# Optimization experiments

Hardware: AMD Instinct MI355X
Metric: run time of the kernel (lower is better)

Reference implementation:

```python
import jax, jax.numpy as jnp
from jax import lax
import numpy as np

V, E, H, T, L = 100000, 300, 512, 11, 4096
START, STOP = 9, 10
NEG_INF = -10000.0


def setup_inputs() -> dict:
    key = jax.random.key(0)
    ks = jax.random.split(key, 14)
    n = lambda k, s, sc=0.1: jax.random.normal(k, s, dtype=jnp.float32) * sc
    transitions = jax.random.normal(ks[12], (T, T), dtype=jnp.float32)
    # __init__ pins transitions into START and out of STOP
    transitions = transitions.at[START, :].set(NEG_INF).at[:, STOP].set(NEG_INF)
    return {
        'sentence': jax.random.randint(ks[0], (L,), 0, V),
        'embedding': n(ks[1], (V, E), 1.0),
        'w_ih_f': n(ks[2], (4 * H, E)), 'w_hh_f': n(ks[3], (4 * H, H)),
        'b_ih_f': n(ks[4], (4 * H,)), 'b_hh_f': n(ks[5], (4 * H,)),
        'w_ih_b': n(ks[6], (4 * H, E)), 'w_hh_b': n(ks[7], (4 * H, H)),
        'b_ih_b': n(ks[8], (4 * H,)), 'b_hh_b': n(ks[9], (4 * H,)),
        'w_tag': n(ks[10], (T, 2 * H)), 'b_tag': n(ks[11], (T,)),
        'transitions': transitions,
    }


def _lstm(x, w_ih, w_hh, b_ih, b_hh, reverse):
    # x: [L, E]; PyTorch gate order i, f, g, o
    Hd = w_hh.shape[1]
    # precompute input projections for all timesteps: [L, 4H]
    xg = x @ w_ih.T + b_ih + b_hh
    def step(carry, xt):
        h, c = carry
        g = xt + w_hh @ h
        i, f, gg, o = jnp.split(g, 4)
        c = jax.nn.sigmoid(f) * c + jax.nn.sigmoid(i) * jnp.tanh(gg)
        h = jax.nn.sigmoid(o) * jnp.tanh(c)
        return (h, c), h
    init = (jnp.zeros((Hd,), x.dtype), jnp.zeros((Hd,), x.dtype))
    _, hs = lax.scan(step, init, xg, reverse=reverse)
    return hs  # [L, H]


def _get_lstm_features(sentence, embedding, w_ih_f, w_hh_f, b_ih_f, b_hh_f,
                       w_ih_b, w_hh_b, b_ih_b, b_hh_b, w_tag, b_tag):
    x = embedding[sentence]  # [L, E]
    hf = _lstm(x, w_ih_f, w_hh_f, b_ih_f, b_hh_f, reverse=False)
    hb = _lstm(x, w_ih_b, w_hh_b, b_ih_b, b_hh_b, reverse=True)
    h = jnp.concatenate([hf, hb], axis=-1)  # [L, 2H]
    return h @ w_tag.T + b_tag  # [L, T]


def _viterbi(feats, transitions):
    init = jnp.full((T,), NEG_INF, feats.dtype).at[START].set(0.0)
    def step(fv, feat):
        scores = fv[None, :] + transitions  # [T_next, T_prev]
        bptr = jnp.argmax(scores, axis=1)
        fv2 = jnp.max(scores, axis=1) + feat
        return fv2, bptr
    fv, bptrs = lax.scan(step, init, feats)  # bptrs: [L, T]
    terminal = fv + transitions[STOP]
    best = jnp.argmax(terminal)
    path_score = terminal[best]
    def back(tag, bp):
        return bp[tag], tag
    _, path = lax.scan(back, best, bptrs, reverse=True)  # tags for t=0..L-1
    return path_score, path


def reference(sentence, embedding, w_ih_f, w_hh_f, b_ih_f, b_hh_f,
              w_ih_b, w_hh_b, b_ih_b, b_hh_b, w_tag, b_tag, transitions):
    feats = _get_lstm_features(sentence, embedding, w_ih_f, w_hh_f, b_ih_f, b_hh_f,
                               w_ih_b, w_hh_b, b_ih_b, b_hh_b, w_tag, b_tag)
    return _viterbi(feats, transitions)
```

## Files before the change

kernel.cpp:

```cpp
#include <hip/hip_runtime.h>
#include <hip/hip_bf16.h>
#include <hip/hip_fp16.h>
#include <stdint.h>

#define LL 4096
#define EE 300
#define HH 512
#define G4H 2048
#define TT 11
#define TSTART 9
#define TSTOP 10
#define NEGINF -10000.0f

typedef unsigned long long u64;
typedef _Float16 h2v __attribute__((ext_vector_type(2)));

__device__ __forceinline__ float sigf(float x){
    x = fminf(fmaxf(x, -30.f), 30.f);
    return 1.0f / (1.0f + __expf(-x));
}
__device__ __forceinline__ float tanhfast(float x){
    x = fminf(fmaxf(x, -15.f), 15.f);
    float e = __expf(-2.0f * x);
    return (1.0f - e) / (1.0f + e);
}
__device__ __forceinline__ u64 lda(const u64* p){
    return __hip_atomic_load(p, __ATOMIC_RELAXED, __HIP_MEMORY_SCOPE_AGENT);
}
__device__ __forceinline__ h2v u2h(unsigned u){
    union { unsigned v; h2v h; } c; c.v = u; return c.h;
}
__device__ __forceinline__ h2v pk(float a, float b){
    auto r = __builtin_amdgcn_cvt_pkrtz(a, b);
    union { decltype(r) x; h2v h; } c; c.x = r; return c.h;
}

__global__ void k0_zero(u64* __restrict__ comm){
    int i = blockIdx.x * blockDim.x + threadIdx.x;
    if (i < 2 * 2 * HH) comm[i] = 0ull;
}

__global__ __launch_bounds__(256) void k1_xg(
    const int* __restrict__ sent, const float* __restrict__ emb,
    const float* __restrict__ wih_f, const float* __restrict__ bih_f, const float* __restrict__ bhh_f,
    const float* __restrict__ wih_b, const float* __restrict__ bih_b, const float* __restrict__ bhh_b,
    float* __restrict__ xg_f, float* __restrict__ xg_b)
{
    __shared__ float elds[32 * 304];
    int t0  = blockIdx.x * 32;
    int r0  = blockIdx.y * 256;
    int dir = blockIdx.z;
    const float* wih = dir ? wih_b : wih_f;
    const float* bih = dir ? bih_b : bih_f;
    const float* bhh = dir ? bhh_b : bhh_f;
    float* xg = dir ? xg_b : xg_f;

    for (int idx = threadIdx.x; idx < 32 * EE; idx += 256){
        int i = idx / EE, e = idx - i * EE;
        elds[i * 304 + e] = emb[(long)sent[t0 + i] * EE + e];
    }
    __syncthreads();

    int rA = r0 + (threadIdx.x & 127);
    int rB = rA + 128;
    int half = threadIdx.x >> 7;
    float accA[16], accB[16];
    #pragma unroll
    for (int i = 0; i < 16; i++){ accA[i] = 0.f; accB[i] = 0.f; }
    const float* wrowA = wih + (long)rA * EE;
    const float* wrowB = wih + (long)rB * EE;
    for (int e4 = 0; e4 < 75; e4++){
        float4 wa = *reinterpret_cast<const float4*>(wrowA + e4 * 4);
        float4 wb = *reinterpret_cast<const float4*>(wrowB + e4 * 4);
        #pragma unroll
        for (int i = 0; i < 16; i++){
            float4 ev = *reinterpret_cast<const float4*>(&elds[(half * 16 + i) * 304 + e4 * 4]);
            accA[i] += wa.x * ev.x + wa.y * ev.y + wa.z * ev.z + wa.w * ev.w;
            accB[i] += wb.x * ev.x + wb.y * ev.y + wb.z * ev.z + wb.w * ev.w;
        }
    }
    float bA = bih[rA] + bhh[rA];
    float bB = bih[rB] + bhh[rB];
    #pragma unroll
    for (int i = 0; i < 16; i++){
        int t = t0 + half * 16 + i;
        xg[(long)t * G4H + rA] = accA[i] + bA;
        xg[(long)t * G4H + rB] = accB[i] + bB;
    }
}

__global__ __launch_bounds__(512) void k2_lstm(
    const float* __restrict__ whh_f, const float* __restrict__ whh_b,
    const float* __restrict__ xg_f, const float* __restrict__ xg_b,
    float* __restrict__ hs_f, float* __restrict__ hs_b,
    u64* __restrict__ comm)
{
    int dir = blockIdx.x >> 5;
    int b   = blockIdx.x & 31;
    int j0  = b * 16;
    int tid = threadIdx.x;
    int w   = tid >> 6;
    int l   = tid & 63;
    int g   = l >> 4;
    int jl  = l & 15;
    int row = g * HH + j0 + jl;

    const float* whh = dir ? whh_b : whh_f;
    const float* xg  = dir ? xg_b  : xg_f;
    float* hs        = dir ? hs_b  : hs_f;
    u64* cm          = comm + dir * 2 * HH;

    h2v wreg[32];
    {
        const float* wp = whh + (size_t)row * HH + w * 64;
        #pragma unroll
        for (int m = 0; m < 32; m += 2){
            float4 v = *reinterpret_cast<const float4*>(wp + 2 * m);
            wreg[m]     = pk(v.x, v.y);
            wreg[m + 1] = pk(v.z, v.w);
        }
    }

    __shared__ __align__(16) unsigned short hl16[2][HH];
    __shared__ float plds[2][512];
    float c = 0.f;

    for (int s = 0; s < LL; ++s){
        int t = dir ? (LL - 1 - s) : s;
        float xgv = 0.f;
        if (tid < 64) xgv = xg[(size_t)t * G4H + row];

        if (s == 0){
            hl16[0][tid] = 0;
        } else {
            const u64* pw = cm + (s & 1) * HH + tid;
            u64 v = lda(pw);
            unsigned want = (unsigned)s;
            while (!__all((unsigned)(v >> 32) == want)){
                if ((unsigned)(v >> 32) != want) v = lda(pw);
            }
            float hval = __uint_as_float((unsigned)v);
            union { h2v h; unsigned u; } cv2; cv2.h = pk(hval, hval);
            hl16[s & 1][tid] = (unsigned short)(cv2.u & 0xFFFFu);
        }
        __syncthreads();

        float a0 = 0.f, a1 = 0.f, a2 = 0.f, a3 = 0.f;
        {
            const uint4* hseg = reinterpret_cast<const uint4*>(&hl16[s & 1][w * 64]);
            #pragma unroll
            for (int q = 0; q < 8; q += 2){
                uint4 h0 = hseg[q];
                uint4 h1 = hseg[q + 1];
                a0 = __builtin_amdgcn_fdot2(wreg[4*q+0], u2h(h0.x), a0, false);
                a1 = __builtin_amdgcn_fdot2(wreg[4*q+1], u2h(h0.y), a1, false);
                a2 = __builtin_amdgcn_fdot2(wreg[4*q+2], u2h(h0.z), a2, false);
                a3 = __builtin_amdgcn_fdot2(wreg[4*q+3], u2h(h0.w), a3, false);
                a0 = __builtin_amdgcn_fdot2(wreg[4*q+4], u2h(h1.x), a0, false);
                a1 = __builtin_amdgcn_fdot2(wreg[4*q+5], u2h(h1.y), a1, false);
                a2 = __builtin_amdgcn_fdot2(wreg[4*q+6], u2h(h1.z), a2, false);
                a3 = __builtin_amdgcn_fdot2(wreg[4*q+7], u2h(h1.w), a3, false);
            }
        }
        plds[s & 1][tid] = (a0 + a1) + (a2 + a3);
        __syncthreads();

        if (w == 0){
            float sum = 0.f;
            #pragma unroll
            for (int q = 0; q < 8; q++) sum += plds[s & 1][q * 64 + l];
            float pre = sum + xgv;
            float vi = __shfl(pre, jl,      64);
            float vf = __shfl(pre, 16 + jl, 64);
            float vg = __shfl(pre, 32 + jl, 64);
            float vo = __shfl(pre, 48 + jl, 64);
            c = sigf(vf) * c + sigf(vi) * tanhfast(vg);
            float h = sigf(vo) * tanhfast(c);
            if (l < 16){
                union { float f; unsigned u; } hv; hv.f = h;
                u64 pk2 = ((u64)(s + 1) << 32) | (u64)hv.u;
                __hip_atomic_store(cm + ((s + 1) & 1) * HH + (j0 + l), pk2,
                                   __ATOMIC_RELAXED, __HIP_MEMORY_SCOPE_AGENT);
                hs[(size_t)t * HH + (j0 + l)] = h;
            }
        }
    }
}

__global__ __launch_bounds__(64) void k3_feats(
    const float* __restrict__ hs_f, const float* __restrict__ hs_b,
    const float* __restrict__ wtag, const float* __restrict__ btag,
    float* __restrict__ feats)
{
    int t = blockIdx.x;
    int lane = threadIdx.x;
    float hreg[16];
    #pragma unroll
    for (int q = 0; q < 16; q++){
        int k = q * 64 + lane;
        hreg[q] = (q < 8) ? hs_f[(long)t * HH + k] : hs_b[(long)t * HH + (k - HH)];
    }
    for (int n = 0; n < TT; n++){
        float a = 0.f;
        #pragma unroll
        for (int q = 0; q < 16; q++){
            a += wtag[n * 1024 + q * 64 + lane] * hreg[q];
        }
        #pragma unroll
        for (int off = 32; off; off >>= 1) a += __shfl_down(a, off, 64);
        if (lane == 0) feats[t * 12 + n] = a + btag[n];
    }
}

__global__ __launch_bounds__(64) void k4a_chunk(
    const float* __restrict__ feats, const float* __restrict__ trans,
    float* __restrict__ Pmat)
{
    int c = blockIdx.x;
    int lane = threadIdx.x;
    float tr[TT][TT];
    #pragma unroll
    for (int n = 0; n < TT; n++)
        #pragma unroll
        for (int p = 0; p < TT; p++) tr[n][p] = trans[n * TT + p];

    float pv[TT];
    #pragma unroll
    for (int n = 0; n < TT; n++) pv[n] = (n == lane) ? 0.f : NEGINF;

    for (int i = 0; i < 64; i++){
        int t = c * 64 + i;
        float ft[TT];
        #pragma unroll
        for (int n = 0; n < TT; n++) ft[n] = feats[t * 12 + n];
        float pn[TT];
        #pragma unroll
        for (int n = 0; n < TT; n++){
            float m = tr[n][0] + pv[0];
            #pragma unroll
            for (int p = 1; p < TT; p++) m = fmaxf(m, tr[n][p] + pv[p]);
            pn[n] = m + ft[n];
        }
        #pragma unroll
        for (int n = 0; n < TT; n++) pv[n] = pn[n];
    }
    if (lane < TT){
        #pragma unroll
        for (int n = 0; n < TT; n++) Pmat[(c * TT + n) * TT + lane] = pv[n];
    }
}

__global__ __launch_bounds__(64) void k4b_bound(
    const float* __restrict__ Pmat, float* __restrict__ fvb)
{
    int lane = threadIdx.x;
    int ln = (lane < TT) ? lane : 0;
    float fv[TT];
    #pragma unroll
    for (int n = 0; n < TT; n++) fv[n] = (n == TSTART) ? 0.f : NEGINF;

    for (int c = 0; c < 64; c++){
        if (lane < TT) fvb[c * TT + lane] = fv[lane];
        float nf = NEGINF;
        #pragma unroll
        for (int s = 0; s < TT; s++)
            nf = fmaxf(nf, Pmat[(c * TT + ln) * TT + s] + fv[s]);
        #pragma unroll
        for (int n = 0; n < TT; n++) fv[n] = __shfl(nf, n, 64);
    }
    if (lane < TT) fvb[64 * TT + lane] = fv[lane];
}

__global__ __launch_bounds__(64) void k4c_bp(
    const float* __restrict__ feats, const float* __restrict__ trans,
    const float* __restrict__ fvb, u64* __restrict__ bpw)
{
    int c = blockIdx.x;
    int lane = threadIdx.x;
    int ln = (lane < TT) ? lane : 0;
    float trl[TT];
    #pragma unroll
    for (int p = 0; p < TT; p++) trl[p] = trans[ln * TT + p];
    float fv[TT];
    #pragma unroll
    for (int n = 0; n < TT; n++) fv[n] = fvb[c * TT + n];

    for (int i = 0; i < 64; i++){
        int t = c * 64 + i;
        float best = NEGINF; int bp = 0;
        #pragma unroll
        for (int p = 0; p < TT; p++){
            float sp = trl[p] + fv[p];
            if (sp > best){ best = sp; bp = p; }
        }
        if (lane >= TT) bp = 0;
        unsigned lo = (lane < 8) ? ((unsigned)bp << (4 * lane)) : 0u;
        unsigned hi = (lane >= 8 && lane < TT) ? ((unsigned)bp << (4 * (lane - 8))) : 0u;
        #pragma unroll
        for (int off = 1; off < 16; off <<= 1){
            lo |= __shfl_xor(lo, off, 16); hi |= __shfl_xor(hi, off, 16);
        }
        if (lane == 0) bpw[t] = (u64)lo | ((u64)hi << 32);
        float nf = (lane < TT) ? best + feats[t * 12 + ln] : NEGINF;
        #pragma unroll
        for (int n = 0; n < TT; n++) fv[n] = __shfl(nf, n, 64);
    }
}

__global__ __launch_bounds__(256) void k4d_bt(
    const u64* __restrict__ bpw, const float* __restrict__ fvb,
    const float* __restrict__ trans, float* __restrict__ out)
{
    __shared__ u64 bl[LL];
    int tid = threadIdx.x;
    for (int i = tid; i < LL; i += 256) bl[i] = bpw[i];
    __syncthreads();

    if (tid < 64){
        int lane = tid;
        int ln = (lane < TT) ? lane : 0;
        float term = (lane < TT) ? (fvb[64 * TT + ln] + trans[TSTOP * TT + ln]) : -3.0e38f;
        int idx = (lane < TT) ? lane : 63;
        #pragma unroll
        for (int off = 32; off; off >>= 1){
            float os = __shfl_down(term, off, 64);
            int   oi = __shfl_down(idx,  off, 64);
            if (os > term || (os == term && oi < idx)){ term = os; idx = oi; }
        }
        if (lane == 0){
            out[0] = term;
            int tag = idx;
            out[1 + (LL - 1)] = (float)tag;
            for (int u = LL - 1; u >= 1; --u){
                tag = (int)((bl[u] >> (4 * tag)) & 15ull);
                out[u] = (float)tag;
            }
        }
    }
}

__global__ void k_dbg(float* out, float v){ out[0] = v; }

extern "C" void kernel_launch(void* const* d_in, const int* in_sizes, int n_in,
                              void* d_out, int out_size, void* d_ws, size_t ws_size,
                              hipStream_t stream)
{
    const int*   sent  = (const int*)  d_in[0];
    const float* emb   = (const float*)d_in[1];
    const float* wih_f = (const float*)d_in[2];
    const float* whh_f = (const float*)d_in[3];
    const float* bih_f = (const float*)d_in[4];
    const float* bhh_f = (const float*)d_in[5];
    const float* wih_b = (const float*)d_in[6];
    const float* whh_b = (const float*)d_in[7];
    const float* bih_b = (const float*)d_in[8];
    const float* bhh_b = (const float*)d_in[9];
    const float* wtag  = (const float*)d_in[10];
    const float* btag  = (const float*)d_in[11];
    const float* trans = (const float*)d_in[12];
    float* out = (float*)d_out;

    char* ws = (char*)d_ws;
    size_t off = 0;
    float* xg_f = (float*)(ws + off); off += (size_t)LL * G4H * 4;
    float* xg_b = (float*)(ws + off); off += (size_t)LL * G4H * 4;
    float* hs_f = (float*)(ws + off); off += (size_t)LL * HH * 4;
    float* hs_b = (float*)(ws + off); off += (size_t)LL * HH * 4;
    float* feats= (float*)(ws + off); off += (size_t)LL * 12 * 4;
    u64* comm   = (u64*)(ws + off);   off += 2 * 2 * HH * 8;
    float* Pmat = (float*)(ws + off); off += (size_t)64 * TT * TT * 4;
    float* fvb  = (float*)(ws + off); off += (size_t)65 * TT * 4 + 64;
    u64* bpw    = (u64*)(ws + off);   off += (size_t)LL * 8;

    if (off > ws_size){
        k_dbg<<<1, 1, 0, stream>>>(out, (float)ws_size);
        return;
    }

    k0_zero<<<8, 256, 0, stream>>>(comm);
    k1_xg<<<dim3(128, 8, 2), 256, 0, stream>>>(sent, emb, wih_f, bih_f, bhh_f,
                                               wih_b, bih_b, bhh_b, xg_f, xg_b);
    k2_lstm<<<64, 512, 0, stream>>>(whh_f, whh_b, xg_f, xg_b, hs_f, hs_b, comm);
    k3_feats<<<LL, 64, 0, stream>>>(hs_f, hs_b, wtag, btag, feats);
    k4a_chunk<<<64, 64, 0, stream>>>(feats, trans, Pmat);
    k4b_bound<<<1, 64, 0, stream>>>(Pmat, fvb);
    k4c_bp<<<64, 64, 0, stream>>>(feats, trans, fvb, bpw);
    k4d_bt<<<1, 256, 0, stream>>>(bpw, fvb, trans, out);
}
```

Measured before the change: 6.633 ms.

## Give each wave whole LSTM units and reduce with shuffles, dropping the LDS barrier

The recurrent step kernel is remapped so each wave owns two hidden units (eight gate rows) over the full K dimension, not a K-slice of all 64 rows. Partial dot products are combined with a transposing xor-shuffle butterfly instead of an LDS partial-sum buffer, so the second __syncthreads per timestep goes away and every wave computes its own gate nonlinearities. The spin-wait on the cross-block h exchange now keeps four outstanding loads in flight to cut polling latency. The cost is more shuffle instructions and redundant activation math across waves.

After: 11.21 ms. 1.69x slower.

```diff
diff --git a/kernel.cpp b/kernel.cpp
--- a/kernel.cpp
+++ b/kernel.cpp
@@ -101,88 +101,98 @@
     int tid = threadIdx.x;
     int w   = tid >> 6;
     int l   = tid & 63;
-    int g   = l >> 4;
-    int jl  = l & 15;
-    int row = g * HH + j0 + jl;
+    int jp  = (l >> 2) & 1;
+    int jA  = j0 + 2 * w;
+    int b0  = l & 1, b1 = (l >> 1) & 1, b2 = jp;
 
     const float* whh = dir ? whh_b : whh_f;
     const float* xg  = dir ? xg_b  : xg_f;
     float* hs        = dir ? hs_b  : hs_f;
     u64* cm          = comm + dir * 2 * HH;
 
-    h2v wreg[32];
-    {
-        const float* wp = whh + (size_t)row * HH + w * 64;
-        #pragma unroll
-        for (int m = 0; m < 32; m += 2){
-            float4 v = *reinterpret_cast<const float4*>(wp + 2 * m);
-            wreg[m]     = pk(v.x, v.y);
-            wreg[m + 1] = pk(v.z, v.w);
-        }
+    h2v wreg[8][4];
+    #pragma unroll
+    for (int r = 0; r < 8; r++){
+        const float* wp = whh + (size_t)((r & 3) * HH + jA + (r >> 2)) * HH + 8 * l;
+        float4 v0 = *reinterpret_cast<const float4*>(wp);
+        float4 v1 = *reinterpret_cast<const float4*>(wp + 4);
+        wreg[r][0] = pk(v0.x, v0.y);
+        wreg[r][1] = pk(v0.z, v0.w);
+        wreg[r][2] = pk(v1.x, v1.y);
+        wreg[r][3] = pk(v1.z, v1.w);
     }
 
     __shared__ __align__(16) unsigned short hl16[2][HH];
-    __shared__ float plds[2][512];
     float c = 0.f;
 
     for (int s = 0; s < LL; ++s){
         int t = dir ? (LL - 1 - s) : s;
-        float xgv = 0.f;
-        if (tid < 64) xgv = xg[(size_t)t * G4H + row];
+        float xgd = xg[(size_t)t * G4H + (l & 3) * HH + jA + jp];
 
         if (s == 0){
             hl16[0][tid] = 0;
         } else {
             const u64* pw = cm + (s & 1) * HH + tid;
-            u64 v = lda(pw);
+            u64 v0 = lda(pw), v1 = lda(pw), v2 = lda(pw), v3 = lda(pw);
             unsigned want = (unsigned)s;
-            while (!__all((unsigned)(v >> 32) == want)){
-                if ((unsigned)(v >> 32) != want) v = lda(pw);
+            while (!__all((unsigned)(v0 >> 32) == want)){
+                v0 = v1; v1 = v2; v2 = v3; v3 = lda(pw);
             }
-            float hval = __uint_as_float((unsigned)v);
+            float hval = __uint_as_float((unsigned)v0);
             union { h2v h; unsigned u; } cv2; cv2.h = pk(hval, hval);
             hl16[s & 1][tid] = (unsigned short)(cv2.u & 0xFFFFu);
         }
         __syncthreads();
 
-        float a0 = 0.f, a1 = 0.f, a2 = 0.f, a3 = 0.f;
-        {
-            const uint4* hseg = reinterpret_cast<const uint4*>(&hl16[s & 1][w * 64]);
-            #pragma unroll
-            for (int q = 0; q < 8; q += 2){
-                uint4 h0 = hseg[q];
-                uint4 h1 = hseg[q + 1];
-                a0 = __builtin_amdgcn_fdot2(wreg[4*q+0], u2h(h0.x), a0, false);
-                a1 = __builtin_amdgcn_fdot2(wreg[4*q+1], u2h(h0.y), a1, false);
-                a2 = __builtin_amdgcn_fdot2(wreg[4*q+2], u2h(h0.z), a2, false);
-                a3 = __builtin_amdgcn_fdot2(wreg[4*q+3], u2h(h0.w), a3, false);
-                a0 = __builtin_amdgcn_fdot2(wreg[4*q+4], u2h(h1.x), a0, false);
-                a1 = __builtin_amdgcn_fdot2(wreg[4*q+5], u2h(h1.y), a1, false);
-                a2 = __builtin_amdgcn_fdot2(wreg[4*q+6], u2h(h1.z), a2, false);
-                a3 = __builtin_amdgcn_fdot2(wreg[4*q+7], u2h(h1.w), a3, false);
-            }
-        }
-        plds[s & 1][tid] = (a0 + a1) + (a2 + a3);
-        __syncthreads();
-
-        if (w == 0){
-            float sum = 0.f;
-            #pragma unroll
-            for (int q = 0; q < 8; q++) sum += plds[s & 1][q * 64 + l];
-            float pre = sum + xgv;
-            float vi = __shfl(pre, jl,      64);
-            float vf = __shfl(pre, 16 + jl, 64);
-            float vg = __shfl(pre, 32 + jl, 64);
-            float vo = __shfl(pre, 48 + jl, 64);
-            c = sigf(vf) * c + sigf(vi) * tanhfast(vg);
-            float h = sigf(vo) * tanhfast(c);
-            if (l < 16){
-                union { float f; unsigned u; } hv; hv.f = h;
-                u64 pk2 = ((u64)(s + 1) << 32) | (u64)hv.u;
-                __hip_atomic_store(cm + ((s + 1) & 1) * HH + (j0 + l), pk2,
-                                   __ATOMIC_RELAXED, __HIP_MEMORY_SCOPE_AGENT);
-                hs[(size_t)t * HH + (j0 + l)] = h;
-            }
+        uint4 hv4 = *reinterpret_cast<const uint4*>(&hl16[s & 1][8 * l]);
+        h2v h0 = u2h(hv4.x), h1 = u2h(hv4.y), h2 = u2h(hv4.z), h3 = u2h(hv4.w);
+
+        float acc[8];
+        #pragma unroll
+        for (int r = 0; r < 8; r++){
+            float a = __builtin_amdgcn_fdot2(wreg[r][0], h0, 0.f,  false);
+            a = __builtin_amdgcn_fdot2(wreg[r][1], h1, a, false);
+            a = __builtin_amdgcn_fdot2(wreg[r][2], h2, a, false);
+            acc[r] = __builtin_amdgcn_fdot2(wreg[r][3], h3, a, false);
+        }
+
+        float t1[4];
+        #pragma unroll
+        for (int m = 0; m < 4; m++){
+            float tx = b0 ? acc[2 * m]     : acc[2 * m + 1];
+            float kp = b0 ? acc[2 * m + 1] : acc[2 * m];
+            t1[m] = kp + __shfl_xor(tx, 1, 64);
+        }
+        float t2[2];
+        #pragma unroll
+        for (int m = 0; m < 2; m++){
+            float tx = b1 ? t1[2 * m]     : t1[2 * m + 1];
+            float kp = b1 ? t1[2 * m + 1] : t1[2 * m];
+            t2[m] = kp + __shfl_xor(tx, 2, 64);
+        }
+        float tx3 = b2 ? t2[0] : t2[1];
+        float kp3 = b2 ? t2[1] : t2[0];
+        float d = kp3 + __shfl_xor(tx3, 4, 64);
+        d += __shfl_xor(d, 8, 64);
+        d += __shfl_xor(d, 16, 64);
+        d += __shfl_xor(d, 32, 64);
+
+        float pre = d + xgd;
+        int base = l & 60;
+        float vi = __shfl(pre, base,     64);
+        float vf = __shfl(pre, base + 1, 64);
+        float vg = __shfl(pre, base + 2, 64);
+        float vo = __shfl(pre, base + 3, 64);
+        c = sigf(vf) * c + sigf(vi) * tanhfast(vg);
+        float hv = sigf(vo) * tanhfast(c);
+
+        if (l == 0 || l == 4){
+            int j = jA + jp;
+            union { float f; unsigned u; } cv; cv.f = hv;
+            u64 pk2 = ((u64)(s + 1) << 32) | (u64)cv.u;
+            __hip_atomic_store(cm + ((s + 1) & 1) * HH + j, pk2,
+                               __ATOMIC_RELAXED, __HIP_MEMORY_SCOPE_AGENT);
+            hs[(size_t)t * HH + j] = hv;
         }
     }
 }
```
